# Kernel tuning notes

Measured on AMD Instinct MI355X. Metric: run time of the kernel, lower is better.

## Reference

```python
import jax, jax.numpy as jnp
import numpy as np

EPI_AGE_PENALTY = 0.02
EPI_MIN_STRENGTH = 0.001
EPI_STRENGTH_BOOST = 0.5
RMS_EPS = 1e-6


def setup_inputs() -> dict:
    key = jax.random.key(0)
    k1, k2, k3, k4, k5, k6 = jax.random.split(key, 6)
    B, S, D = 32, 8192, 512
    return {
        "q_win": jax.random.normal(k1, (B, D), dtype=jnp.float32),
        "epi_keys": jax.random.normal(k2, (B, S, D), dtype=jnp.float32),
        "epi_vals": jax.random.normal(k3, (B, S, D), dtype=jnp.float32),
        "epi_age": jax.random.uniform(k4, (B, S), dtype=jnp.float32),
        "epi_strength": jax.random.uniform(k5, (B, S), dtype=jnp.float32),
        "scale": jnp.ones((D,), dtype=jnp.float32),  # RMSNorm learned scale
    }


def reference(q_win, epi_keys, epi_vals, epi_age, epi_strength, scale):
    # L2-normalize query [B,D] and keys [B,S,D]
    qn = q_win / (jnp.linalg.norm(q_win, axis=-1, keepdims=True) + 1e-6)
    kn = epi_keys / (jnp.linalg.norm(epi_keys, axis=-1, keepdims=True) + 1e-6)
    # cosine similarity [B,S]
    sim = jnp.einsum("bsd,bd->bs", kn, qn)
    str_log = jnp.log(jnp.clip(epi_strength, EPI_MIN_STRENGTH, 1e9))
    logits = sim + EPI_STRENGTH_BOOST * str_log - EPI_AGE_PENALTY * epi_age
    alive = (epi_strength > EPI_MIN_STRENGTH).astype(jnp.float32)
    logits = logits + (alive - 1.0) * 1000.0
    w = jax.nn.softmax(logits, axis=-1)
    # softmax-weighted read over slots -> [B,D]
    read = jnp.einsum("bs,bsd->bd", w, epi_vals)
    # RMSNorm
    rms = jnp.sqrt(jnp.mean(jnp.square(read), axis=-1, keepdims=True) + RMS_EPS)
    read = read / rms * scale
    return (read, w, logits)
```

## Files before the change

kernel.cpp:

```cpp
#include <hip/hip_runtime.h>
#include <math.h>

#define BB 32
#define SS 8192
#define DD 512
#define D4 (DD / 4)

static constexpr float AGE_PEN = 0.02f;
static constexpr float MIN_STR = 0.001f;
static constexpr float STR_BOOST = 0.5f;
static constexpr float RMS_EPS_F = 1e-6f;

__device__ inline float block_sum(float v, volatile float* red) {
    int tid = threadIdx.x, lane = tid & 63, wid = tid >> 6;
#pragma unroll
    for (int off = 32; off; off >>= 1) v += __shfl_xor(v, off);
    if (lane == 0) red[wid] = v;
    __syncthreads();
    if (tid == 0) {
        float t = 0.f;
        int nw = blockDim.x >> 6;
        for (int i = 0; i < nw; i++) t += red[i];
        red[0] = t;
    }
    __syncthreads();
    float r = red[0];
    __syncthreads();
    return r;
}

__device__ inline float block_max(float v, volatile float* red) {
    int tid = threadIdx.x, lane = tid & 63, wid = tid >> 6;
#pragma unroll
    for (int off = 32; off; off >>= 1) v = fmaxf(v, __shfl_xor(v, off));
    if (lane == 0) red[wid] = v;
    __syncthreads();
    if (tid == 0) {
        float t = -1e30f;
        int nw = blockDim.x >> 6;
        for (int i = 0; i < nw; i++) t = fmaxf(t, red[i]);
        red[0] = t;
    }
    __syncthreads();
    float r = red[0];
    __syncthreads();
    return r;
}

__global__ __launch_bounds__(256) void qn_kernel(const float* __restrict__ q,
                                                 float* __restrict__ qn) {
    __shared__ float red[8];
    int b = blockIdx.x, tid = threadIdx.x;
    const float* row = q + b * DD;
    float v0 = row[tid], v1 = row[tid + 256];
    float ss = block_sum(v0 * v0 + v1 * v1, red);
    float inv = 1.f / (sqrtf(ss) + 1e-6f);
    qn[b * DD + tid] = v0 * inv;
    qn[b * DD + tid + 256] = v1 * inv;
}

__global__ __launch_bounds__(256) void logits_kernel(const float4* __restrict__ keys,
                                                     const float* __restrict__ qn,
                                                     const float* __restrict__ age,
                                                     const float* __restrict__ strength,
                                                     float* __restrict__ logits) {
    int wid = threadIdx.x >> 6, lane = threadIdx.x & 63;
    int row = blockIdx.x * 4 + wid;
    int b = row >> 13;
    const float4* k = keys + (long long)row * D4;
    const float4* q4 = (const float4*)qn + b * D4;

    float4 k0 = k[lane], k1 = k[lane + 64];
    float4 q0 = q4[lane], q1 = q4[lane + 64];

    float kk = k0.x * k0.x + k0.y * k0.y + k0.z * k0.z + k0.w * k0.w +
               k1.x * k1.x + k1.y * k1.y + k1.z * k1.z + k1.w * k1.w;
    float kq = k0.x * q0.x + k0.y * q0.y + k0.z * q0.z + k0.w * q0.w +
               k1.x * q1.x + k1.y * q1.y + k1.z * q1.z + k1.w * q1.w;
#pragma unroll
    for (int off = 32; off; off >>= 1) {
        kk += __shfl_xor(kk, off);
        kq += __shfl_xor(kq, off);
    }
    if (lane == 0) {
        float st = strength[row];
        float a = age[row];
        float sim = kq / (sqrtf(kk) + 1e-6f);
        float lg = sim + STR_BOOST * logf(fminf(fmaxf(st, MIN_STR), 1e9f)) - AGE_PEN * a;
        if (!(st > MIN_STR)) lg -= 1000.f;
        logits[row] = lg;
    }
}

__global__ __launch_bounds__(256) void softmax_kernel(const float* __restrict__ logits,
                                                      float* __restrict__ w) {
    __shared__ float red[8];
    int b = blockIdx.x, tid = threadIdx.x;
    const float4* lg4 = (const float4*)(logits + b * SS);
    float4* w4 = (float4*)(w + b * SS);

    float4 loc[8];
    float mx = -1e30f;
#pragma unroll
    for (int i = 0; i < 8; i++) {
        float4 v = lg4[tid + i * 256];
        loc[i] = v;
        mx = fmaxf(mx, fmaxf(fmaxf(v.x, v.y), fmaxf(v.z, v.w)));
    }
    mx = block_max(mx, red);

    float sum = 0.f;
#pragma unroll
    for (int i = 0; i < 8; i++) {
        float4 v = loc[i];
        v.x = expf(v.x - mx);
        v.y = expf(v.y - mx);
        v.z = expf(v.z - mx);
        v.w = expf(v.w - mx);
        sum += v.x + v.y + v.z + v.w;
        loc[i] = v;
    }
    sum = block_sum(sum, red);
    float inv = 1.f / sum;
#pragma unroll
    for (int i = 0; i < 8; i++) {
        float4 v = loc[i];
        v.x *= inv; v.y *= inv; v.z *= inv; v.w *= inv;
        w4[tid + i * 256] = v;
    }
}

__global__ __launch_bounds__(128) void wsum_kernel(const float4* __restrict__ vals,
                                                   const float* __restrict__ w,
                                                   float4* __restrict__ partial) {
    __shared__ float sw[128];
    int chunk = blockIdx.x, b = blockIdx.y, tid = threadIdx.x;
    int s0 = chunk * 128;
    sw[tid] = w[b * SS + s0 + tid];
    __syncthreads();

    const float4* vbase = vals + ((long long)b * SS + s0) * D4 + tid;
    float4 acc = {0.f, 0.f, 0.f, 0.f};
#pragma unroll 4
    for (int s = 0; s < 128; s++) {
        float4 v = vbase[(long long)s * D4];
        float ww = sw[s];
        acc.x += ww * v.x;
        acc.y += ww * v.y;
        acc.z += ww * v.z;
        acc.w += ww * v.w;
    }
    partial[(b * 64 + chunk) * D4 + tid] = acc;
}

__global__ __launch_bounds__(256) void reduce_rms_kernel(const float* __restrict__ partial,
                                                         const float* __restrict__ scale,
                                                         float* __restrict__ readout) {
    __shared__ float red[8];
    int b = blockIdx.x, tid = threadIdx.x;
    const float* p = partial + (long long)b * 64 * DD;
    float r0 = 0.f, r1 = 0.f;
#pragma unroll 4
    for (int c = 0; c < 64; c++) {
        r0 += p[c * DD + tid];
        r1 += p[c * DD + tid + 256];
    }
    float ss = block_sum(r0 * r0 + r1 * r1, red);
    float rms = sqrtf(ss / (float)DD + RMS_EPS_F);
    float inv = 1.f / rms;
    readout[b * DD + tid] = r0 * inv * scale[tid];
    readout[b * DD + tid + 256] = r1 * inv * scale[tid + 256];
}

extern "C" void kernel_launch(void* const* d_in, const int* in_sizes, int n_in,
                              void* d_out, int out_size, void* d_ws, size_t ws_size,
                              hipStream_t stream) {
    const float* q        = (const float*)d_in[0];
    const float* keys     = (const float*)d_in[1];
    const float* vals     = (const float*)d_in[2];
    const float* age      = (const float*)d_in[3];
    const float* strength = (const float*)d_in[4];
    const float* scale    = (const float*)d_in[5];

    float* out = (float*)d_out;
    float* readout = out;
    float* w       = out + BB * DD;
    float* logits  = out + BB * DD + BB * SS;

    float* ws = (float*)d_ws;
    float* qn = ws;
    float* partial = ws + BB * DD;

    qn_kernel<<<BB, 256, 0, stream>>>(q, qn);
    logits_kernel<<<BB * SS / 4, 256, 0, stream>>>((const float4*)keys, qn, age, strength, logits);
    softmax_kernel<<<BB, 256, 0, stream>>>(logits, w);
    wsum_kernel<<<dim3(64, BB), 128, 0, stream>>>((const float4*)vals, w, (float4*)partial);
    reduce_rms_kernel<<<BB, 256, 0, stream>>>(partial, scale, readout);
}
```

Baseline: 203.0 us.

## Fuse logits, exp, and value-weighted sum into one pass without max subtraction

Merges query normalization, logits, softmax numerator and the weighted value sum into a single kernel, so keys and values are streamed together in one pass. The softmax max subtraction is dropped because logits are bounded (cosine plus log strength), and normalization by the summed exponentials moves into the reduce kernel. A small kernel then rebuilds the weights from the logits. This removes a kernel launch, the extra logits and weights round trips, and the serial per-batch softmax. The cost is relying on the logits never overflowing exp, and each block now covers only 128 rows.

New measurement: 221.5 us. 1.09x slower.

```diff
diff --git a/kernel.cpp b/kernel.cpp
--- a/kernel.cpp
+++ b/kernel.cpp
@@ -5,11 +5,17 @@
 #define SS 8192
 #define DD 512
 #define D4 (DD / 4)
+#define CHUNKS 64
+#define CHUNK 128
 
 static constexpr float AGE_PEN = 0.02f;
 static constexpr float MIN_STR = 0.001f;
 static constexpr float STR_BOOST = 0.5f;
 static constexpr float RMS_EPS_F = 1e-6f;
+
+__device__ inline float dot4(float4 a, float4 b) {
+    return a.x * b.x + a.y * b.y + a.z * b.z + a.w * b.w;
+}
 
 __device__ inline float block_sum(float v, volatile float* red) {
     int tid = threadIdx.x, lane = tid & 63, wid = tid >> 6;
@@ -17,159 +23,122 @@
     for (int off = 32; off; off >>= 1) v += __shfl_xor(v, off);
     if (lane == 0) red[wid] = v;
     __syncthreads();
-    if (tid == 0) {
-        float t = 0.f;
-        int nw = blockDim.x >> 6;
-        for (int i = 0; i < nw; i++) t += red[i];
-        red[0] = t;
-    }
-    __syncthreads();
-    float r = red[0];
+    float r = red[0] + red[1] + red[2] + red[3];
     __syncthreads();
     return r;
 }
 
-__device__ inline float block_max(float v, volatile float* red) {
-    int tid = threadIdx.x, lane = tid & 63, wid = tid >> 6;
+__global__ __launch_bounds__(256) void fused_kernel(
+    const float4* __restrict__ keys, const float4* __restrict__ vals,
+    const float* __restrict__ q, const float* __restrict__ age,
+    const float* __restrict__ strength, float* __restrict__ logits,
+    float4* __restrict__ partial, float* __restrict__ esum_partial) {
+    __shared__ float4 racc[4 * D4];
+    __shared__ float rede[4];
+
+    int chunk = blockIdx.x, b = blockIdx.y;
+    int tid = threadIdx.x, wid = tid >> 6, lane = tid & 63;
+
+    const float4* q4 = (const float4*)q + b * D4;
+    float4 q0 = q4[lane], q1 = q4[lane + 64];
+    float qq = dot4(q0, q0) + dot4(q1, q1);
 #pragma unroll
-    for (int off = 32; off; off >>= 1) v = fmaxf(v, __shfl_xor(v, off));
-    if (lane == 0) red[wid] = v;
-    __syncthreads();
-    if (tid == 0) {
-        float t = -1e30f;
-        int nw = blockDim.x >> 6;
-        for (int i = 0; i < nw; i++) t = fmaxf(t, red[i]);
-        red[0] = t;
-    }
-    __syncthreads();
-    float r = red[0];
-    __syncthreads();
-    return r;
-}
+    for (int off = 32; off; off >>= 1) qq += __shfl_xor(qq, off);
+    float qinv = 1.f / (sqrtf(qq) + 1e-6f);
+    q0.x *= qinv; q0.y *= qinv; q0.z *= qinv; q0.w *= qinv;
+    q1.x *= qinv; q1.y *= qinv; q1.z *= qinv; q1.w *= qinv;
 
-__global__ __launch_bounds__(256) void qn_kernel(const float* __restrict__ q,
-                                                 float* __restrict__ qn) {
-    __shared__ float red[8];
-    int b = blockIdx.x, tid = threadIdx.x;
-    const float* row = q + b * DD;
-    float v0 = row[tid], v1 = row[tid + 256];
-    float ss = block_sum(v0 * v0 + v1 * v1, red);
-    float inv = 1.f / (sqrtf(ss) + 1e-6f);
-    qn[b * DD + tid] = v0 * inv;
-    qn[b * DD + tid + 256] = v1 * inv;
-}
+    long long s0 = (long long)b * SS + chunk * CHUNK;
+    float4 acc0 = {0.f, 0.f, 0.f, 0.f}, acc1 = {0.f, 0.f, 0.f, 0.f};
+    float esum = 0.f;
 
-__global__ __launch_bounds__(256) void logits_kernel(const float4* __restrict__ keys,
-                                                     const float* __restrict__ qn,
-                                                     const float* __restrict__ age,
-                                                     const float* __restrict__ strength,
-                                                     float* __restrict__ logits) {
-    int wid = threadIdx.x >> 6, lane = threadIdx.x & 63;
-    int row = blockIdx.x * 4 + wid;
-    int b = row >> 13;
-    const float4* k = keys + (long long)row * D4;
-    const float4* q4 = (const float4*)qn + b * D4;
+#pragma unroll 2
+    for (int s = wid; s < CHUNK; s += 4) {
+        long long row = s0 + s;
+        const float4* k = keys + row * D4;
+        const float4* v = vals + row * D4;
+        float4 k0 = k[lane], k1 = k[lane + 64];
+        float4 v0 = v[lane], v1 = v[lane + 64];
 
-    float4 k0 = k[lane], k1 = k[lane + 64];
-    float4 q0 = q4[lane], q1 = q4[lane + 64];
-
-    float kk = k0.x * k0.x + k0.y * k0.y + k0.z * k0.z + k0.w * k0.w +
-               k1.x * k1.x + k1.y * k1.y + k1.z * k1.z + k1.w * k1.w;
-    float kq = k0.x * q0.x + k0.y * q0.y + k0.z * q0.z + k0.w * q0.w +
-               k1.x * q1.x + k1.y * q1.y + k1.z * q1.z + k1.w * q1.w;
+        float kk = dot4(k0, k0) + dot4(k1, k1);
+        float kq = dot4(k0, q0) + dot4(k1, q1);
 #pragma unroll
-    for (int off = 32; off; off >>= 1) {
-        kk += __shfl_xor(kk, off);
-        kq += __shfl_xor(kq, off);
-    }
-    if (lane == 0) {
+        for (int off = 32; off; off >>= 1) {
+            kk += __shfl_xor(kk, off);
+            kq += __shfl_xor(kq, off);
+        }
         float st = strength[row];
         float a = age[row];
-        float sim = kq / (sqrtf(kk) + 1e-6f);
-        float lg = sim + STR_BOOST * logf(fminf(fmaxf(st, MIN_STR), 1e9f)) - AGE_PEN * a;
+        float lg = kq / (sqrtf(kk) + 1e-6f)
+                 + STR_BOOST * logf(fminf(fmaxf(st, MIN_STR), 1e9f))
+                 - AGE_PEN * a;
         if (!(st > MIN_STR)) lg -= 1000.f;
-        logits[row] = lg;
+        if (lane == 0) logits[row] = lg;
+
+        float e = expf(lg);
+        esum += e;
+        acc0.x += e * v0.x; acc0.y += e * v0.y; acc0.z += e * v0.z; acc0.w += e * v0.w;
+        acc1.x += e * v1.x; acc1.y += e * v1.y; acc1.z += e * v1.z; acc1.w += e * v1.w;
+    }
+
+    racc[wid * D4 + lane] = acc0;
+    racc[wid * D4 + 64 + lane] = acc1;
+    if (lane == 0) rede[wid] = esum;
+    __syncthreads();
+
+    if (tid < D4) {
+        float4 a0 = racc[tid], a1 = racc[D4 + tid], a2 = racc[2 * D4 + tid], a3 = racc[3 * D4 + tid];
+        float4 r;
+        r.x = a0.x + a1.x + a2.x + a3.x;
+        r.y = a0.y + a1.y + a2.y + a3.y;
+        r.z = a0.z + a1.z + a2.z + a3.z;
+        r.w = a0.w + a1.w + a2.w + a3.w;
+        partial[((long long)b * CHUNKS + chunk) * D4 + tid] = r;
+    } else if (tid == D4) {
+        esum_partial[b * CHUNKS + chunk] = rede[0] + rede[1] + rede[2] + rede[3];
     }
 }
 
-__global__ __launch_bounds__(256) void softmax_kernel(const float* __restrict__ logits,
-                                                      float* __restrict__ w) {
-    __shared__ float red[8];
+__global__ __launch_bounds__(256) void reduce_rms_kernel(
+    const float* __restrict__ partial, const float* __restrict__ esum_partial,
+    const float* __restrict__ scale, float* __restrict__ readout,
+    float* __restrict__ inv_esum) {
+    __shared__ float red[4];
     int b = blockIdx.x, tid = threadIdx.x;
-    const float4* lg4 = (const float4*)(logits + b * SS);
-    float4* w4 = (float4*)(w + b * SS);
 
-    float4 loc[8];
-    float mx = -1e30f;
-#pragma unroll
-    for (int i = 0; i < 8; i++) {
-        float4 v = lg4[tid + i * 256];
-        loc[i] = v;
-        mx = fmaxf(mx, fmaxf(fmaxf(v.x, v.y), fmaxf(v.z, v.w)));
-    }
-    mx = block_max(mx, red);
-
-    float sum = 0.f;
-#pragma unroll
-    for (int i = 0; i < 8; i++) {
-        float4 v = loc[i];
-        v.x = expf(v.x - mx);
-        v.y = expf(v.y - mx);
-        v.z = expf(v.z - mx);
-        v.w = expf(v.w - mx);
-        sum += v.x + v.y + v.z + v.w;
-        loc[i] = v;
-    }
-    sum = block_sum(sum, red);
-    float inv = 1.f / sum;
-#pragma unroll
-    for (int i = 0; i < 8; i++) {
-        float4 v = loc[i];
-        v.x *= inv; v.y *= inv; v.z *= inv; v.w *= inv;
-        w4[tid + i * 256] = v;
-    }
-}
-
-__global__ __launch_bounds__(128) void wsum_kernel(const float4* __restrict__ vals,
-                                                   const float* __restrict__ w,
-                                                   float4* __restrict__ partial) {
-    __shared__ float sw[128];
-    int chunk = blockIdx.x, b = blockIdx.y, tid = threadIdx.x;
-    int s0 = chunk * 128;
-    sw[tid] = w[b * SS + s0 + tid];
-    __syncthreads();
-
-    const float4* vbase = vals + ((long long)b * SS + s0) * D4 + tid;
-    float4 acc = {0.f, 0.f, 0.f, 0.f};
-#pragma unroll 4
-    for (int s = 0; s < 128; s++) {
-        float4 v = vbase[(long long)s * D4];
-        float ww = sw[s];
-        acc.x += ww * v.x;
-        acc.y += ww * v.y;
-        acc.z += ww * v.z;
-        acc.w += ww * v.w;
-    }
-    partial[(b * 64 + chunk) * D4 + tid] = acc;
-}
-
-__global__ __launch_bounds__(256) void reduce_rms_kernel(const float* __restrict__ partial,
-                                                         const float* __restrict__ scale,
-                                                         float* __restrict__ readout) {
-    __shared__ float red[8];
-    int b = blockIdx.x, tid = threadIdx.x;
-    const float* p = partial + (long long)b * 64 * DD;
+    const float* p = partial + (long long)b * CHUNKS * DD;
     float r0 = 0.f, r1 = 0.f;
 #pragma unroll 4
-    for (int c = 0; c < 64; c++) {
+    for (int c = 0; c < CHUNKS; c++) {
         r0 += p[c * DD + tid];
         r1 += p[c * DD + tid + 256];
     }
+    float le = (tid < CHUNKS) ? esum_partial[b * CHUNKS + tid] : 0.f;
+    float etot = block_sum(le, red);
+    float inv_e = 1.f / etot;
+    if (tid == 0) inv_esum[b] = inv_e;
+    r0 *= inv_e;
+    r1 *= inv_e;
     float ss = block_sum(r0 * r0 + r1 * r1, red);
     float rms = sqrtf(ss / (float)DD + RMS_EPS_F);
     float inv = 1.f / rms;
     readout[b * DD + tid] = r0 * inv * scale[tid];
     readout[b * DD + tid + 256] = r1 * inv * scale[tid + 256];
+}
+
+__global__ __launch_bounds__(256) void w_kernel(const float4* __restrict__ logits,
+                                                const float* __restrict__ inv_esum,
+                                                float4* __restrict__ w) {
+    int i4 = blockIdx.x * 256 + threadIdx.x;
+    int b = i4 >> 11;
+    float inv = inv_esum[b];
+    float4 lg = logits[i4];
+    float4 r;
+    r.x = expf(lg.x) * inv;
+    r.y = expf(lg.y) * inv;
+    r.z = expf(lg.z) * inv;
+    r.w = expf(lg.w) * inv;
+    w[i4] = r;
 }
 
 extern "C" void kernel_launch(void* const* d_in, const int* in_sizes, int n_in,
@@ -188,12 +157,13 @@
     float* logits  = out + BB * DD + BB * SS;
 
     float* ws = (float*)d_ws;
-    float* qn = ws;
-    float* partial = ws + BB * DD;
+    float* partial      = ws;
+    float* esum_partial = ws + BB * CHUNKS * DD;
+    float* inv_esum     = esum_partial + BB * CHUNKS;
 
-    qn_kernel<<<BB, 256, 0, stream>>>(q, qn);
-    logits_kernel<<<BB * SS / 4, 256, 0, stream>>>((const float4*)keys, qn, age, strength, logits);
-    softmax_kernel<<<BB, 256, 0, stream>>>(logits, w);
-    wsum_kernel<<<dim3(64, BB), 128, 0, stream>>>((const float4*)vals, w, (float4*)partial);
-    reduce_rms_kernel<<<BB, 256, 0, stream>>>(partial, scale, readout);
+    fused_kernel<<<dim3(CHUNKS, BB), 256, 0, stream>>>(
+        (const float4*)keys, (const float4*)vals, q, age, strength,
+        logits, (float4*)partial, esum_partial);
+    reduce_rms_kernel<<<BB, 256, 0, stream>>>(partial, esum_partial, scale, readout, inv_esum);
+    w_kernel<<<BB * SS / 4 / 256, 256, 0, stream>>>((const float4*)logits, inv_esum, (float4*)w);
 }
```
